# Optimization experiments

Measured on AMD Instinct MI355X. Metric: run time of the kernel, lower is better.

## Reference

```python
import jax, jax.numpy as jnp
import numpy as np

B, N, F, H, D = 4096, 14, 768, 1, 768  # batch, num_diseases, feature_dim, num_heads, hidden_dim
L = 3  # number of GAT layers


def setup_inputs() -> dict:
    key = jax.random.key(0)
    ks = jax.random.split(key, 8)
    features = jax.random.normal(ks[0], (B, N, F), dtype=jnp.float32)
    # random adjacency mask; ensure nonzero diagonal so no row is fully masked
    mask = (jax.random.uniform(ks[1], (B, N, N)) > 0.3).astype(jnp.float32)
    adj = jnp.maximum(mask, jnp.eye(N, dtype=jnp.float32))
    W_emb = jax.random.normal(ks[2], (F, D), dtype=jnp.float32) / np.sqrt(F)
    b_emb = jnp.zeros((D,), dtype=jnp.float32)
    gat_W = jax.random.normal(ks[3], (L, D, H * D), dtype=jnp.float32) / np.sqrt(D)
    gat_a = jax.random.normal(ks[4], (L, 2 * D, H), dtype=jnp.float32) / np.sqrt(2 * D)
    W_out = jax.random.normal(ks[5], (H * D, F), dtype=jnp.float32) / np.sqrt(H * D)
    b_out = jnp.zeros((F,), dtype=jnp.float32)
    return dict(features=features, adj=adj, W_emb=W_emb, b_emb=b_emb,
                gat_W=gat_W, gat_a=gat_a, W_out=W_out, b_out=b_out)


def _gat_layer(x, adj, W, a):
    # x: [B, N, D], W: [D, H*D], a: [2D, H]
    Bm, Nn = x.shape[0], x.shape[1]
    Wh = (x @ W).reshape(Bm, Nn, H, D)
    # e[b,i,j,h] = Wh[b,i,h] . a[:D,h] + Wh[b,j,h] . a[D:,h]  (concat attention, un-materialized)
    a_i, a_j = a[:D], a[D:]
    ei = jnp.einsum('bnhd,dh->bnh', Wh, a_i)
    ej = jnp.einsum('bnhd,dh->bnh', Wh, a_j)
    e = ei[:, :, None, :] + ej[:, None, :, :]  # [B, N, N, H]
    e = jnp.where(adj[..., None] > 0, e, jnp.float32(-1e30))  # masked_fill(-inf)
    attn = jax.nn.softmax(e, axis=2)  # softmax over j (dim=2), matches torch
    h = jnp.einsum('bijh,bjhd->bihd', attn, Wh)  # attention-weighted aggregation
    return h.reshape(Bm, Nn, H * D), attn  # concat=True output


def reference(features, adj, W_emb, b_emb, gat_W, gat_a, W_out, b_out):
    # dropout layers are identity at inference
    x = features @ W_emb + b_emb  # disease_embedding
    attns = []
    for l in range(L):
        x, attn = _gat_layer(x, adj, gat_W[l], gat_a[l])
        attns.append(attn)
        if l < L - 1:
            x = jax.nn.elu(x)
    out = x @ W_out + b_out  # output_proj
    return (out, attns[0], attns[1], attns[2])
```

## Files before the change

kernel.cpp:

```cpp
#include <hip/hip_runtime.h>

typedef unsigned short u16;
typedef float f32x16 __attribute__((ext_vector_type(16)));
typedef short bf16x8 __attribute__((ext_vector_type(8)));
typedef unsigned short u16x8 __attribute__((ext_vector_type(8)));

#define ND 768
#define KD 768

__device__ __forceinline__ float bf2f(u16 u) {
    union { unsigned i; float f; } v; v.i = ((unsigned)u) << 16; return v.f;
}
__device__ __forceinline__ u16 f2bf(float f) {
    union { float f; unsigned u; } x; x.f = f;
    unsigned r = x.u + 0x7fffu + ((x.u >> 16) & 1u);
    return (u16)(r >> 16);
}
__device__ __forceinline__ void async16(const void* g, void* l) {
    __builtin_amdgcn_global_load_lds((const __attribute__((address_space(1))) void*)g,
                                     (__attribute__((address_space(3))) void*)l, 16, 0, 0);
}

__global__ __launch_bounds__(256) void mega_prep(const float* __restrict__ W_emb,
                                                 const float* __restrict__ gat_W,
                                                 const float* __restrict__ W_out,
                                                 const float4* __restrict__ features,
                                                 u16* __restrict__ Wt,
                                                 u16* __restrict__ WeBf,
                                                 u16* __restrict__ W3Bf,
                                                 u16* __restrict__ H0)
{
    __shared__ float lds[64][65];
    const int blk = blockIdx.x;
    const int tid = threadIdx.x;
    if (blk < 432) {
        const int mi = blk / 144;
        const int mm = (mi == 0) ? 1 : (mi == 1) ? 2 : 4;
        const float* src = (mm == 4) ? W_out : gat_W + (size_t)(mm - 1) * 589824;
        const int r  = blk % 144;
        const int tr = r / 12, tc = r % 12;
        const int c  = tid & 63, w4 = tid >> 6;
        #pragma unroll
        for (int i = 0; i < 16; ++i) {
            int kk = i * 4 + w4;
            lds[kk][c] = src[(size_t)(tr * 64 + kk) * 768 + tc * 64 + c];
        }
        __syncthreads();
        u16* dst = Wt + (size_t)mm * 589824;
        #pragma unroll
        for (int i = 0; i < 16; ++i) {
            int nn = i * 4 + w4;
            dst[(size_t)(tc * 64 + nn) * 768 + tr * 64 + c] = f2bf(lds[c][nn]);
        }
    } else if (blk < 1584) {
        int bi = blk - 432;
        const float4* src;
        u16* dst;
        if (bi < 576) { src = (const float4*)W_emb; dst = WeBf; }
        else          { src = (const float4*)(gat_W + 2 * 589824); dst = W3Bf; bi -= 576; }
        const int i = bi * 256 + tid;
        float4 v = src[i];
        union { u16 s[4]; uint2 u; } o;
        o.s[0] = f2bf(v.x); o.s[1] = f2bf(v.y); o.s[2] = f2bf(v.z); o.s[3] = f2bf(v.w);
        ((uint2*)dst)[i] = o.u;
    } else {
        for (int i = (blk - 1584) * 256 + tid; i < 11010048; i += 4096 * 256) {
            float4 v = features[i];
            union { u16 s[4]; uint2 u; } o;
            o.s[0] = f2bf(v.x); o.s[1] = f2bf(v.y); o.s[2] = f2bf(v.z); o.s[3] = f2bf(v.w);
            ((uint2*)H0)[i] = o.u;
        }
    }
}

__global__ __launch_bounds__(256) void prep_vecs2(const float* __restrict__ W3,
                                                  const float* __restrict__ ga2,
                                                  const float* __restrict__ be,
                                                  const u16* __restrict__ Wt1,
                                                  float* __restrict__ w3ai,
                                                  float* __restrict__ w3aj,
                                                  float* __restrict__ bfus)
{
    const int lane = threadIdx.x & 63;
    const int d = blockIdx.x * 4 + (threadIdx.x >> 6);
    const float* row = W3 + (size_t)d * 768;
    const u16* wrow = Wt1 + (size_t)d * 768;
    float ai = 0.f, aj = 0.f, bf = 0.f;
    for (int j = lane; j < 768; j += 64) {
        float w = row[j];
        ai += w * ga2[j];
        aj += w * ga2[768 + j];
        bf += be[j] * bf2f(wrow[j]);
    }
    #pragma unroll
    for (int off = 32; off; off >>= 1) {
        ai += __shfl_down(ai, off);
        aj += __shfl_down(aj, off);
        bf += __shfl_down(bf, off);
    }
    if (lane == 0) { w3ai[d] = ai; w3aj[d] = aj; bfus[d] = bf; }
}

template<bool F32OUT, bool SWZ>
__global__ __launch_bounds__(256) void gemm_bt(const u16* __restrict__ A,
                                               const u16* __restrict__ A2,
                                               const u16* __restrict__ Bt,
                                               const u16* __restrict__ Bt2,
                                               const float* __restrict__ bias,
                                               void* __restrict__ Cout)
{
    __shared__ u16 lds3[3][2][4096];
    const int tid  = threadIdx.x;
    const int lane = tid & 63;
    const int wvb  = tid & ~63;
    const int wm   = ((tid >> 7) & 1) * 64;
    const int wn   = ((tid >> 6) & 1) * 64;
    const int wg = blockIdx.x;
    const int id = SWZ ? ((wg & 7) * 336 + (wg >> 3)) : wg;
    const int tn = (id % 6) * 128;
    const int tm = (id / 6) * 128;
    const bool hi = (A2 != nullptr) && (tm >= 768);
    const u16* AU  = hi ? A2 : A;
    const u16* BtU = hi ? Bt2 : Bt;
    const int tmA  = hi ? tm - 768 : tm;

    f32x16 acc[2][2] = {};

    const int r31 = lane & 31;
    const int l5  = lane >> 5;
    const int key = (r31 >> 1) & 3;

    const int row0 = tid >> 2;
    const int kc0  = (((tid & 3) ^ ((tid >> 3) & 3)) << 3);
    const u16* aSrc = AU  + (size_t)(tmA + row0) * KD + kc0;
    const u16* bSrc = BtU + (size_t)(tn + row0) * KD + kc0;

    #define STAGE(b, ks_) { const int k0 = (ks_) * 32;                       \
        async16(aSrc + k0,                   &lds3[b][0][wvb * 8]);          \
        async16(aSrc + (size_t)64 * KD + k0, &lds3[b][0][(256 + wvb) * 8]);  \
        async16(bSrc + k0,                   &lds3[b][1][wvb * 8]);          \
        async16(bSrc + (size_t)64 * KD + k0, &lds3[b][1][(256 + wvb) * 8]); }

    STAGE(0, 0);
    STAGE(1, 1);

    #pragma unroll 3
    for (int ks = 0; ks < KD / 32; ++ks) {
        const int cur = ks % 3;
        if (ks < KD / 32 - 1)
            asm volatile("s_waitcnt vmcnt(4)" ::: "memory");
        else
            asm volatile("s_waitcnt vmcnt(0)" ::: "memory");
        __builtin_amdgcn_s_barrier();
        asm volatile("" ::: "memory");
        if (ks + 2 < KD / 32) STAGE((ks + 2) % 3, ks + 2);

        const u16* As = lds3[cur][0];
        const u16* Bs = lds3[cur][1];
        bf16x8 af[2][2], bf[2][2];
        #pragma unroll
        for (int fr = 0; fr < 2; ++fr)
            #pragma unroll
            for (int ka = 0; ka < 2; ++ka) {
                int chA = ((ka * 2 + l5) ^ key) << 3;
                af[fr][ka] = *(const bf16x8*)&As[(wm + fr * 32 + r31) * 32 + chA];
                bf[fr][ka] = *(const bf16x8*)&Bs[(wn + fr * 32 + r31) * 32 + chA];
            }
        #pragma unroll
        for (int fr = 0; fr < 2; ++fr)
            #pragma unroll
            for (int fc = 0; fc < 2; ++fc)
                #pragma unroll
                for (int ka = 0; ka < 2; ++ka)
                    acc[fr][fc] = __builtin_amdgcn_mfma_f32_32x32x16_bf16(
                        af[fr][ka], bf[fc][ka], acc[fr][fc], 0, 0, 0);
    }
    #undef STAGE

    #pragma unroll
    for (int fc = 0; fc < 2; ++fc) {
        int col = tn + wn + fc * 32 + r31;
        float bv = bias ? bias[col] : 0.0f;
        #pragma unroll
        for (int fr = 0; fr < 2; ++fr) {
            int rowb = tm + wm + fr * 32 + 4 * l5;
            #pragma unroll
            for (int reg = 0; reg < 16; ++reg) {
                int row = rowb + (reg & 3) + 8 * (reg >> 2);
                float v = acc[fr][fc][reg] + bv;
                if (F32OUT)
                    ((float*)Cout)[(size_t)row * ND + col] = v;
                else
                    ((u16*)Cout)[(size_t)row * ND + col] = f2bf(v);
            }
        }
    }
}

template<bool ELU, bool DOTS>
__global__ __launch_bounds__(256) void gat_mix(const u16* __restrict__ Wh,
                                               const float* __restrict__ adj,
                                               const float* __restrict__ avec,
                                               float* __restrict__ attn_out,
                                               u16* __restrict__ Xout,
                                               const float* __restrict__ w3ai,
                                               const float* __restrict__ w3aj,
                                               float* __restrict__ eiOut,
                                               float* __restrict__ ejOut)
{
    __shared__ u16 wh[14 * 768];
    __shared__ float s_ei[14], s_ej[14];
    __shared__ float s_attn[196];
    __shared__ float s_dots[14][2];
    const int b = blockIdx.x;
    const int tid = threadIdx.x;
    const u16* whb = Wh + (size_t)b * 10752;

    if (DOTS && tid < 28) ((float*)s_dots)[tid] = 0.f;
    for (int c = tid; c < 1344; c += 256)
        ((uint4*)wh)[c] = ((const uint4*)whb)[c];
    __syncthreads();

    if (tid < 224) {
        const int i = tid >> 4, l = tid & 15;
        float ai = 0.f, aj = 0.f;
        #pragma unroll
        for (int c = 0; c < 6; ++c) {
            int d = c * 128 + l * 8;
            u16x8 v  = *(const u16x8*)&wh[i * 768 + d];
            float4 x0 = *(const float4*)&avec[d];
            float4 x1 = *(const float4*)&avec[d + 4];
            float4 y0 = *(const float4*)&avec[768 + d];
            float4 y1 = *(const float4*)&avec[768 + d + 4];
            float w0 = bf2f(v[0]), w1 = bf2f(v[1]), w2 = bf2f(v[2]), w3 = bf2f(v[3]);
            float w4 = bf2f(v[4]), w5 = bf2f(v[5]), w6 = bf2f(v[6]), w7 = bf2f(v[7]);
            ai += w0*x0.x + w1*x0.y + w2*x0.z + w3*x0.w + w4*x1.x + w5*x1.y + w6*x1.z + w7*x1.w;
            aj += w0*y0.x + w1*y0.y + w2*y0.z + w3*y0.w + w4*y1.x + w5*y1.y + w6*y1.z + w7*y1.w;
        }
        #pragma unroll
        for (int off = 8; off; off >>= 1) {
            ai += __shfl_xor(ai, off);
            aj += __shfl_xor(aj, off);
        }
        if (l == 0) { s_ei[i] = ai; s_ej[i] = aj; }
    }
    __syncthreads();

    if (tid < 14) {
        const int i = tid;
        float e[14];
        float mx = -3.0e38f;
        #pragma unroll
        for (int j = 0; j < 14; ++j) {
            float ev = (adj[(size_t)b * 196 + i * 14 + j] > 0.f) ? (s_ei[i] + s_ej[j]) : -1.0e30f;
            e[j] = ev; mx = fmaxf(mx, ev);
        }
        float sum = 0.f;
        #pragma unroll
        for (int j = 0; j < 14; ++j) { float pp = __expf(e[j] - mx); e[j] = pp; sum += pp; }
        float inv = 1.0f / sum;
        #pragma unroll
        for (int j = 0; j < 14; ++j) s_attn[i * 14 + j] = e[j] * inv;
    }
    __syncthreads();

    if (tid < 196) attn_out[(size_t)b * 196 + tid] = s_attn[tid];

    for (int pp = tid; pp < 14 * 48; pp += 256) {
        const int i  = pp / 48;
        const int d0 = (pp % 48) * 16;
        float acc[16] = {};
        #pragma unroll
        for (int j = 0; j < 14; ++j) {
            float aw = s_attn[i * 14 + j];
            u16x8 wv0 = *(const u16x8*)&wh[j * 768 + d0];
            u16x8 wv1 = *(const u16x8*)&wh[j * 768 + d0 + 8];
            #pragma unroll
            for (int qq = 0; qq < 8; ++qq) {
                acc[qq]     += aw * bf2f(wv0[qq]);
                acc[8 + qq] += aw * bf2f(wv1[qq]);
            }
        }
        float pi = 0.f, pj = 0.f;
        union { u16 s[16]; uint4 u[2]; } o;
        #pragma unroll
        for (int qq = 0; qq < 16; ++qq) {
            float v = acc[qq];
            if (ELU && v < 0.f) v = __expf(v) - 1.0f;
            if (DOTS) { pi += v * w3ai[d0 + qq]; pj += v * w3aj[d0 + qq]; }
            o.s[qq] = f2bf(v);
        }
        if (DOTS) {
            atomicAdd(&s_dots[i][0], pi);
            atomicAdd(&s_dots[i][1], pj);
        }
        *(uint4*)&Xout[(size_t)b * 10752 + i * 768 + d0]     = o.u[0];
        *(uint4*)&Xout[(size_t)b * 10752 + i * 768 + d0 + 8] = o.u[1];
    }
    if (DOTS) {
        __syncthreads();
        if (tid < 14) {
            eiOut[(size_t)b * 14 + tid] = s_dots[tid][0];
            ejOut[(size_t)b * 14 + tid] = s_dots[tid][1];
        }
    }
}

__global__ __launch_bounds__(256) void gat_out(const u16* __restrict__ Z,
                                               const float* __restrict__ adj,
                                               const float* __restrict__ eiG,
                                               const float* __restrict__ ejG,
                                               const float* __restrict__ b_out,
                                               float* __restrict__ attn_out,
                                               float* __restrict__ outp)
{
    __shared__ u16 wh[14 * 768];
    __shared__ float s_attn[196];
    const int b = blockIdx.x;
    const int tid = threadIdx.x;
    const u16* zb = Z + (size_t)b * 10752;

    for (int c = tid; c < 1344; c += 256)
        ((uint4*)wh)[c] = ((const uint4*)zb)[c];

    if (tid < 14) {
        const int i = tid;
        float ei = eiG[(size_t)b * 14 + i];
        float e[14];
        float mx = -3.0e38f;
        #pragma unroll
        for (int j = 0; j < 14; ++j) {
            float ev = (adj[(size_t)b * 196 + i * 14 + j] > 0.f)
                           ? (ei + ejG[(size_t)b * 14 + j]) : -1.0e30f;
            e[j] = ev; mx = fmaxf(mx, ev);
        }
        float sum = 0.f;
        #pragma unroll
        for (int j = 0; j < 14; ++j) { float pp = __expf(e[j] - mx); e[j] = pp; sum += pp; }
        float inv = 1.0f / sum;
        #pragma unroll
        for (int j = 0; j < 14; ++j) s_attn[i * 14 + j] = e[j] * inv;
    }
    __syncthreads();

    if (tid < 196) attn_out[(size_t)b * 196 + tid] = s_attn[tid];

    for (int pp = tid; pp < 14 * 48; pp += 256) {
        const int i  = pp / 48;
        const int d0 = (pp % 48) * 16;
        float acc[16];
        #pragma unroll
        for (int qq = 0; qq < 16; ++qq) acc[qq] = b_out[d0 + qq];
        #pragma unroll
        for (int j = 0; j < 14; ++j) {
            float aw = s_attn[i * 14 + j];
            u16x8 wv0 = *(const u16x8*)&wh[j * 768 + d0];
            u16x8 wv1 = *(const u16x8*)&wh[j * 768 + d0 + 8];
            #pragma unroll
            for (int qq = 0; qq < 8; ++qq) {
                acc[qq]     += aw * bf2f(wv0[qq]);
                acc[8 + qq] += aw * bf2f(wv1[qq]);
            }
        }
        float* dst = &outp[(size_t)b * 10752 + i * 768 + d0];
        *(float4*)(dst)      = *(float4*)&acc[0];
        *(float4*)(dst + 4)  = *(float4*)&acc[4];
        *(float4*)(dst + 8)  = *(float4*)&acc[8];
        *(float4*)(dst + 12) = *(float4*)&acc[12];
    }
}

extern "C" void kernel_launch(void* const* d_in, const int* in_sizes, int n_in,
                              void* d_out, int out_size, void* d_ws, size_t ws_size,
                              hipStream_t stream)
{
    const float* features = (const float*)d_in[0];
    const float* adj      = (const float*)d_in[1];
    const float* W_emb    = (const float*)d_in[2];
    const float* b_emb    = (const float*)d_in[3];
    const float* gat_W    = (const float*)d_in[4];
    const float* gat_a    = (const float*)d_in[5];
    const float* W_out    = (const float*)d_in[6];
    const float* b_out    = (const float*)d_in[7];
    float* out = (float*)d_out;

    u16* Wh = (u16*)d_ws;
    u16* Wt = Wh + 44040192;
    float* w3ai = (float*)(Wt + 7 * 589824);
    float* w3aj = w3ai + 768;
    float* bfus = w3aj + 768;
    float* eiG  = bfus + 768;
    float* ejG  = eiG + 57344;
    u16* H0 = (u16*)d_out;
    u16* H1 = H0 + 44040192;
    u16* WeBf = H1;
    u16* W3Bf = H1 + 589824;
    float* attn0 = out + 44040192;
    float* attn1 = attn0 + 802816;
    float* attn2 = attn1 + 802816;

    mega_prep<<<dim3(5680), 256, 0, stream>>>(W_emb, gat_W, W_out,
                                              (const float4*)features,
                                              Wt, WeBf, W3Bf, H0);
    prep_vecs2<<<dim3(192), 256, 0, stream>>>(gat_W + 2 * 589824, gat_a + 2 * 1536, b_emb,
                                              Wt + 589824, w3ai, w3aj, bfus);
    gemm_bt<false, false><<<dim3(72), 256, 0, stream>>>(
        Wt + 1 * 589824, Wt + 4 * 589824, WeBf, W3Bf, nullptr, Wt + 5 * 589824);

    dim3 gg(2688);
    gemm_bt<false, true><<<gg, 256, 0, stream>>>(
        H0, nullptr, Wt + 5 * 589824, nullptr, bfus, Wh);
    gat_mix<true, false><<<dim3(4096), 256, 0, stream>>>(Wh, adj, gat_a, attn0, H1,
                                                         nullptr, nullptr, nullptr, nullptr);
    gemm_bt<false, true><<<gg, 256, 0, stream>>>(
        H1, nullptr, Wt + 2 * 589824, nullptr, nullptr, Wh);
    gat_mix<true, true><<<dim3(4096), 256, 0, stream>>>(Wh, adj, gat_a + 1536, attn1, H0,
                                                        w3ai, w3aj, eiG, ejG);
    gemm_bt<false, true><<<gg, 256, 0, stream>>>(
        H0, nullptr, Wt + 6 * 589824, nullptr, nullptr, Wh);
    gat_out<<<dim3(4096), 256, 0, stream>>>(Wh, adj, eiG, ejG, b_out, attn2, out);
}
```

Measured before the change: 593.8 us.

## Fuse feature bf16 conversion into first GEMM and merge vector prep into mega_prep

```diff
diff --git a/kernel.cpp b/kernel.cpp
--- a/kernel.cpp
+++ b/kernel.cpp
@@ -24,11 +24,14 @@
 __global__ __launch_bounds__(256) void mega_prep(const float* __restrict__ W_emb,
                                                  const float* __restrict__ gat_W,
                                                  const float* __restrict__ W_out,
-                                                 const float4* __restrict__ features,
+                                                 const float* __restrict__ gat_a,
+                                                 const float* __restrict__ be,
                                                  u16* __restrict__ Wt,
                                                  u16* __restrict__ WeBf,
                                                  u16* __restrict__ W3Bf,
-                                                 u16* __restrict__ H0)
+                                                 float* __restrict__ w3ai,
+                                                 float* __restrict__ w3aj,
+                                                 float* __restrict__ bfus)
 {
     __shared__ float lds[64][65];
     const int blk = blockIdx.x;
@@ -64,41 +67,26 @@
         o.s[0] = f2bf(v.x); o.s[1] = f2bf(v.y); o.s[2] = f2bf(v.z); o.s[3] = f2bf(v.w);
         ((uint2*)dst)[i] = o.u;
     } else {
-        for (int i = (blk - 1584) * 256 + tid; i < 11010048; i += 4096 * 256) {
-            float4 v = features[i];
-            union { u16 s[4]; uint2 u; } o;
-            o.s[0] = f2bf(v.x); o.s[1] = f2bf(v.y); o.s[2] = f2bf(v.z); o.s[3] = f2bf(v.w);
-            ((uint2*)H0)[i] = o.u;
-        }
-    }
-}
-
-__global__ __launch_bounds__(256) void prep_vecs2(const float* __restrict__ W3,
-                                                  const float* __restrict__ ga2,
-                                                  const float* __restrict__ be,
-                                                  const u16* __restrict__ Wt1,
-                                                  float* __restrict__ w3ai,
-                                                  float* __restrict__ w3aj,
-                                                  float* __restrict__ bfus)
-{
-    const int lane = threadIdx.x & 63;
-    const int d = blockIdx.x * 4 + (threadIdx.x >> 6);
-    const float* row = W3 + (size_t)d * 768;
-    const u16* wrow = Wt1 + (size_t)d * 768;
-    float ai = 0.f, aj = 0.f, bf = 0.f;
-    for (int j = lane; j < 768; j += 64) {
-        float w = row[j];
-        ai += w * ga2[j];
-        aj += w * ga2[768 + j];
-        bf += be[j] * bf2f(wrow[j]);
-    }
-    #pragma unroll
-    for (int off = 32; off; off >>= 1) {
-        ai += __shfl_down(ai, off);
-        aj += __shfl_down(aj, off);
-        bf += __shfl_down(bf, off);
-    }
-    if (lane == 0) { w3ai[d] = ai; w3aj[d] = aj; bfus[d] = bf; }
+        const int lane = tid & 63;
+        const int d = (blk - 1584) * 4 + (tid >> 6);
+        const float* w3row = gat_W + 2 * 589824 + (size_t)d * 768;
+        const float* ga2   = gat_a + 2 * 1536;
+        const float* W1    = gat_W;
+        float ai = 0.f, aj = 0.f, bf = 0.f;
+        for (int j = lane; j < 768; j += 64) {
+            float w = w3row[j];
+            ai += w * ga2[j];
+            aj += w * ga2[768 + j];
+            bf += be[j] * bf2f(f2bf(W1[(size_t)j * 768 + d]));
+        }
+        #pragma unroll
+        for (int off = 32; off; off >>= 1) {
+            ai += __shfl_down(ai, off);
+            aj += __shfl_down(aj, off);
+            bf += __shfl_down(bf, off);
+        }
+        if (lane == 0) { w3ai[d] = ai; w3aj[d] = aj; bfus[d] = bf; }
+    }
 }
 
 template<bool F32OUT, bool SWZ>
@@ -197,6 +185,112 @@
     }
 }
 
+template<bool SWZ>
+__global__ __launch_bounds__(256) void gemm_a32(const float* __restrict__ A,
+                                                const u16* __restrict__ Bt,
+                                                const float* __restrict__ bias,
+                                                u16* __restrict__ Cout)
+{
+    __shared__ float ldsA[3][4096];
+    __shared__ u16   ldsB[3][4096];
+    const int tid  = threadIdx.x;
+    const int lane = tid & 63;
+    const int wvb  = tid & ~63;
+    const int wm   = ((tid >> 7) & 1) * 64;
+    const int wn   = ((tid >> 6) & 1) * 64;
+    const int wg = blockIdx.x;
+    const int id = SWZ ? ((wg & 7) * 336 + (wg >> 3)) : wg;
+    const int tn = (id % 6) * 128;
+    const int tm = (id / 6) * 128;
+
+    f32x16 acc[2][2] = {};
+
+    const int r31 = lane & 31;
+    const int l5  = lane >> 5;
+    const int key = (r31 >> 1) & 3;
+    const int k7  = r31 & 7;
+
+    const int row0 = tid >> 2;
+    const int kc0  = (((tid & 3) ^ ((tid >> 3) & 3)) << 3);
+    const u16* bSrc = Bt + (size_t)(tn + row0) * KD + kc0;
+    const float* aS0; const float* aS1; const float* aS2; const float* aS3;
+    {
+        int c0 = tid, c1 = 256 + tid, c2 = 512 + tid, c3 = 768 + tid;
+        aS0 = A + (size_t)(tm + (c0 >> 3)) * KD + (((c0 & 7) ^ ((c0 >> 3) & 7)) << 2);
+        aS1 = A + (size_t)(tm + (c1 >> 3)) * KD + (((c1 & 7) ^ ((c1 >> 3) & 7)) << 2);
+        aS2 = A + (size_t)(tm + (c2 >> 3)) * KD + (((c2 & 7) ^ ((c2 >> 3) & 7)) << 2);
+        aS3 = A + (size_t)(tm + (c3 >> 3)) * KD + (((c3 & 7) ^ ((c3 >> 3) & 7)) << 2);
+    }
+
+    #define STAGE(b, ks_) { const int k0 = (ks_) * 32;                        \
+        async16(aS0 + k0, &((u16*)ldsA[b])[(wvb) * 8]);                       \
+        async16(aS1 + k0, &((u16*)ldsA[b])[(256 + wvb) * 8]);                 \
+        async16(aS2 + k0, &((u16*)ldsA[b])[(512 + wvb) * 8]);                 \
+        async16(aS3 + k0, &((u16*)ldsA[b])[(768 + wvb) * 8]);                 \
+        async16(bSrc + k0,                   &ldsB[b][wvb * 8]);              \
+        async16(bSrc + (size_t)64 * KD + k0, &ldsB[b][(256 + wvb) * 8]); }
+
+    STAGE(0, 0);
+    STAGE(1, 1);
+
+    #pragma unroll 3
+    for (int ks = 0; ks < KD / 32; ++ks) {
+        const int cur = ks % 3;
+        if (ks < KD / 32 - 1)
+            asm volatile("s_waitcnt vmcnt(6)" ::: "memory");
+        else
+            asm volatile("s_waitcnt vmcnt(0)" ::: "memory");
+        __builtin_amdgcn_s_barrier();
+        asm volatile("" ::: "memory");
+        if (ks + 2 < KD / 32) STAGE((ks + 2) % 3, ks + 2);
+
+        const float* As = ldsA[cur];
+        const u16*   Bs = ldsB[cur];
+        bf16x8 af[2][2], bf[2][2];
+        #pragma unroll
+        for (int fr = 0; fr < 2; ++fr)
+            #pragma unroll
+            for (int ka = 0; ka < 2; ++ka) {
+                const int rA = (wm + fr * 32 + r31) * 32;
+                const int l0 = (ka * 2 + l5) * 2;
+                float4 f0 = *(const float4*)&As[rA + ((l0 ^ k7) << 2)];
+                float4 f1 = *(const float4*)&As[rA + (((l0 + 1) ^ k7) << 2)];
+                union { u16 s[8]; bf16x8 v; } pk;
+                pk.s[0] = f2bf(f0.x); pk.s[1] = f2bf(f0.y);
+                pk.s[2] = f2bf(f0.z); pk.s[3] = f2bf(f0.w);
+                pk.s[4] = f2bf(f1.x); pk.s[5] = f2bf(f1.y);
+                pk.s[6] = f2bf(f1.z); pk.s[7] = f2bf(f1.w);
+                af[fr][ka] = pk.v;
+                int chB = ((ka * 2 + l5) ^ key) << 3;
+                bf[fr][ka] = *(const bf16x8*)&Bs[(wn + fr * 32 + r31) * 32 + chB];
+            }
+        #pragma unroll
+        for (int fr = 0; fr < 2; ++fr)
+            #pragma unroll
+            for (int fc = 0; fc < 2; ++fc)
+                #pragma unroll
+                for (int ka = 0; ka < 2; ++ka)
+                    acc[fr][fc] = __builtin_amdgcn_mfma_f32_32x32x16_bf16(
+                        af[fr][ka], bf[fc][ka], acc[fr][fc], 0, 0, 0);
+    }
+    #undef STAGE
+
+    #pragma unroll
+    for (int fc = 0; fc < 2; ++fc) {
+        int col = tn + wn + fc * 32 + r31;
+        float bv = bias ? bias[col] : 0.0f;
+        #pragma unroll
+        for (int fr = 0; fr < 2; ++fr) {
+            int rowb = tm + wm + fr * 32 + 4 * l5;
+            #pragma unroll
+            for (int reg = 0; reg < 16; ++reg) {
+                int row = rowb + (reg & 3) + 8 * (reg >> 2);
+                Cout[(size_t)row * ND + col] = f2bf(acc[fr][fc][reg] + bv);
+            }
+        }
+    }
+}
+
 template<bool ELU, bool DOTS>
 __global__ __launch_bounds__(256) void gat_mix(const u16* __restrict__ Wh,
                                                const float* __restrict__ adj,
@@ -399,17 +493,13 @@
     float* attn1 = attn0 + 802816;
     float* attn2 = attn1 + 802816;
 
-    mega_prep<<<dim3(5680), 256, 0, stream>>>(W_emb, gat_W, W_out,
-                                              (const float4*)features,
-                                              Wt, WeBf, W3Bf, H0);
-    prep_vecs2<<<dim3(192), 256, 0, stream>>>(gat_W + 2 * 589824, gat_a + 2 * 1536, b_emb,
-                                              Wt + 589824, w3ai, w3aj, bfus);
+    mega_prep<<<dim3(1776), 256, 0, stream>>>(W_emb, gat_W, W_out, gat_a, b_emb,
+                                              Wt, WeBf, W3Bf, w3ai, w3aj, bfus);
     gemm_bt<false, false><<<dim3(72), 256, 0, stream>>>(
         Wt + 1 * 589824, Wt + 4 * 589824, WeBf, W3Bf, nullptr, Wt + 5 * 589824);
 
     dim3 gg(2688);
-    gemm_bt<false, true><<<gg, 256, 0, stream>>>(
-        H0, nullptr, Wt + 5 * 589824, nullptr, bfus, Wh);
+    gemm_a32<true><<<gg, 256, 0, stream>>>(features, Wt + 5 * 589824, bfus, Wh);
     gat_mix<true, false><<<dim3(4096), 256, 0, stream>>>(Wh, adj, gat_a, attn0, H1,
                                                          nullptr, nullptr, nullptr, nullptr);
     gemm_bt<false, true><<<gg, 256, 0, stream>>>(
```

Measured after the change: 662.8 us. 1.12x slower.
